# Kernel tuning notes

Hardware: AMD Instinct MI355X
Metric: run time of the kernel (lower is better)

## Reference

```python
import jax, jax.numpy as jnp
import numpy as np

D = 1024      # total input features
R = 32        # number of ragged regions
RMAX = 32     # max region size (padding target)
HIDDEN = [128, 128]
H1, H2 = HIDDEN
B = 8192      # batch size


def _made_masks(r, rmax, hidden):
    """TFP AutoregressiveNetwork masks (left-to-right order, 'equal' hidden degrees,
    params=2, use_bias=False), zero-padded to rmax features."""
    order = np.arange(1, r + 1)
    degs = [order]
    for u in hidden:
        mn = min(int(degs[-1].min()), r - 1)
        degs.append(np.maximum(mn, np.ceil(np.arange(1, u + 1) * (r - 1) / float(u + 1)).astype(np.int64)))
    m1 = np.zeros((rmax, hidden[0]), bool)
    m1[:r] = degs[0][:, None] <= degs[1][None, :]
    m2 = degs[1][:, None] <= degs[2][None, :]
    mout = np.zeros((hidden[-1], rmax * 2), bool)
    out_deg = np.repeat(order, 2)  # output layout is feature-major: [feat, param]
    mout[:, :2 * r] = degs[-1][:, None] < out_deg[None, :]
    return m1, m2, mout


def setup_inputs() -> dict:
    rng = np.random.default_rng(0)
    perm = rng.permutation(D)
    sizes = rng.integers(8, RMAX + 1, size=R)
    idx = np.zeros((R, RMAX), np.int64)
    valid = np.zeros((R, RMAX), bool)
    M1 = np.zeros((R, RMAX, H1), bool)
    M2 = np.zeros((R, H1, H2), bool)
    Mout = np.zeros((R, H2, RMAX * 2), bool)
    pos = 0
    for i in range(R):
        s = int(sizes[i])
        idx[i, :s] = perm[pos:pos + s]
        pos += s
        valid[i, :s] = True
        M1[i], M2[i], Mout[i] = _made_masks(s, RMAX, HIDDEN)
    key = jax.random.key(0)
    k1, k2, k3, k4 = jax.random.split(key, 4)
    inputs = jax.random.normal(k1, (B, D), jnp.float32)
    W1 = jax.random.normal(k2, (R, RMAX, H1), jnp.float32) / np.float32(np.sqrt(RMAX))
    W2 = jax.random.normal(k3, (R, H1, H2), jnp.float32) / np.float32(np.sqrt(H1))
    Wout = jax.random.normal(k4, (R, H2, RMAX * 2), jnp.float32) / np.float32(np.sqrt(H2))
    return {"inputs": inputs, "W1": W1, "W2": W2, "Wout": Wout,
            "idx": jnp.asarray(idx), "valid": jnp.asarray(valid),
            "M1": jnp.asarray(M1), "M2": jnp.asarray(M2), "Mout": jnp.asarray(Mout)}


def reference(inputs, W1, W2, Wout, idx, valid, M1, M2, Mout):
    f = inputs.dtype
    v = valid.astype(f)                              # [R, RMAX]
    xg = jnp.take(inputs, idx, axis=1) * v           # [B, R, RMAX] ragged gather (padded)
    # MADE masked MLP (relu, no bias), batched over all regions at once
    h1 = jax.nn.relu(jnp.einsum('brd,rdh->brh', xg, W1 * M1.astype(f)))
    h2 = jax.nn.relu(jnp.einsum('brh,rhk->brk', h1, W2 * M2.astype(f)))
    out = jnp.einsum('brk,rko->bro', h2, Wout * Mout.astype(f))
    out = out.reshape(out.shape[0], out.shape[1], RMAX, 2)
    shift, log_s = out[..., 0], out[..., 1]
    # MAF inverse: u = (x - shift) * exp(-log_scale); logdet = -sum(log_scale)
    u = (xg - shift) * jnp.exp(-log_s)
    elem = -0.5 * u * u - 0.5 * jnp.log(2.0 * jnp.pi) - log_s
    ll = jnp.sum(elem * v, axis=-1)                  # [B, R]
    return ll[..., None]                             # [B, R, 1] as in tf.stack of expand_dims
```

## Files before the change

### kernel.cpp

```cpp
#include <hip/hip_runtime.h>
#include <math.h>


#define RR 32
#define DD 1024
#define HH 128
#define OO 64
#define TROWS 32
#define TILES_PER_BLOCK 16
#define BLOCKS_PER_R 16

#define SHP 136
#define SXG 40
#define SXF 38
#define SSC 132

typedef short bf16x8_t __attribute__((ext_vector_type(8)));
typedef float f32x4_t __attribute__((ext_vector_type(4)));
typedef unsigned short u16;
typedef unsigned int u32;

__device__ __forceinline__ u16 bf16_rne(float x) {
    u32 u = __float_as_uint(x);
    u += 0x7FFFu + ((u >> 16) & 1u);
    return (u16)(u >> 16);
}
__device__ __forceinline__ float bf16_tof(u16 h) {
    return __uint_as_float(((u32)h) << 16);
}
__device__ __forceinline__ u16 lo_trunc(float v, u16 h) {
    return (u16)(__float_as_uint(v - bf16_tof(h)) >> 16);
}
__device__ __forceinline__ u32 pack_split(float v) {
    u16 h = bf16_rne(v);
    return (u32)h | ((u32)lo_trunc(v, h) << 16);
}
__device__ __forceinline__ void unpack8(const u32* p, bf16x8_t& hi, bf16x8_t& lo) {
    uint4 a = *reinterpret_cast<const uint4*>(p);
    uint4 b = *reinterpret_cast<const uint4*>(p + 4);
    union { u32 u[4]; bf16x8_t v; } H, L;
    H.u[0] = __builtin_amdgcn_perm(a.y, a.x, 0x05040100u);
    H.u[1] = __builtin_amdgcn_perm(a.w, a.z, 0x05040100u);
    H.u[2] = __builtin_amdgcn_perm(b.y, b.x, 0x05040100u);
    H.u[3] = __builtin_amdgcn_perm(b.w, b.z, 0x05040100u);
    L.u[0] = __builtin_amdgcn_perm(a.y, a.x, 0x07060302u);
    L.u[1] = __builtin_amdgcn_perm(a.w, a.z, 0x07060302u);
    L.u[2] = __builtin_amdgcn_perm(b.y, b.x, 0x07060302u);
    L.u[3] = __builtin_amdgcn_perm(b.w, b.z, 0x07060302u);
    hi = H.v; lo = L.v;
}
__device__ __forceinline__ f32x4_t mfma16(bf16x8_t a, bf16x8_t b, f32x4_t c) {
    return __builtin_amdgcn_mfma_f32_16x16x32_bf16(a, b, c, 0, 0, 0);
}

__device__ __forceinline__ void stage_block(const float* __restrict__ W,
                                            const int* __restrict__ M,
                                            int ldc, int c0, int K, u32* dst, int sd,
                                            int tid)
{
    const int kb = tid >> 3;
    const int cb = tid & 7;
    if (kb * 4 >= K) return;
    const int k0 = kb * 4;
    float e[4][4];
#pragma unroll
    for (int i = 0; i < 4; ++i) {
        const int o = ((k0 + i) * ldc + c0 + 4 * cb) >> 2;
        float4 w = ((const float4*)W)[o];
        int4   m = ((const int4*)M)[o];
        e[i][0] = m.x ? w.x : 0.f; e[i][1] = m.y ? w.y : 0.f;
        e[i][2] = m.z ? w.z : 0.f; e[i][3] = m.w ? w.w : 0.f;
    }
#pragma unroll
    for (int j = 0; j < 4; ++j) {
        uint4 p;
        p.x = pack_split(e[0][j]); p.y = pack_split(e[1][j]);
        p.z = pack_split(e[2][j]); p.w = pack_split(e[3][j]);
        *(uint4*)&dst[(4 * cb + j) * sd + k0] = p;
    }
}

__global__ __launch_bounds__(256, 2)
void made_flow_r9(const float* __restrict__ inputs,
                  const float* __restrict__ W1,
                  const float* __restrict__ W2,
                  const float* __restrict__ Wout,
                  const int* __restrict__ idx,
                  const int* __restrict__ valid,
                  const int* __restrict__ M1,
                  const int* __restrict__ M2,
                  const int* __restrict__ Mout,
                  float* __restrict__ out)
{
    __shared__ __align__(16) char regA[TROWS * SHP * 2 * 2];
    __shared__ __align__(16) char regB[TROWS * SHP * 2 * 2];
    __shared__ __align__(16) u16  xgh[2][TROWS * SXG];
    __shared__ __align__(16) u16  xgl[2][TROWS * SXG];
    __shared__ __align__(16) float xgf[2][TROWS * SXF];
    __shared__ __align__(16) float red_all[TILES_PER_BLOCK][TROWS][4];
    __shared__ int   idx_s[RR];
    __shared__ float v_s[RR];

    u16* const h1h = (u16*)regA;
    u16* const h1l = h1h + TROWS * SHP;
    u32* const scr = (u32*)regA;
    u16* const h2h = (u16*)regB;
    u16* const h2l = h2h + TROWS * SHP;

    const int tid  = threadIdx.x;
    const int r    = blockIdx.x / BLOCKS_PER_R;
    const int rb   = blockIdx.x % BLOCKS_PER_R;
    const int lane = tid & 63;
    const int wave = tid >> 6;
    const int q    = lane >> 4;
    const int l16  = lane & 15;

    if (tid < RR) {
        idx_s[tid] = idx[r * RR + tid];
        v_s[tid]   = valid[r * RR + tid] ? 1.f : 0.f;
    }

    bf16x8_t a1h[2], a1l[2];
    bf16x8_t a2h[2][4], a2l[2][4];
    bf16x8_t aoh[4],    aol[4];
    {
        const float* W1r = W1 + r * RR * HH;   const int* M1r = M1 + r * RR * HH;
        const float* W2r = W2 + r * HH * HH;   const int* M2r = M2 + r * HH * HH;
        const float* Wor = Wout + r * HH * OO; const int* Mor = Mout + r * HH * OO;
        for (int c = 0; c < 4; ++c) {
            __syncthreads();
            stage_block(W2r, M2r, HH, 32 * c, HH, scr, SSC, tid);
            __syncthreads();
            if (wave == c) {
#pragma unroll
                for (int mi = 0; mi < 2; ++mi)
#pragma unroll
                    for (int ks = 0; ks < 4; ++ks)
                        unpack8(&scr[(16 * mi + l16) * SSC + ks * 32 + q * 8],
                                a2h[mi][ks], a2l[mi][ks]);
            }
        }
        for (int c = 0; c < 2; ++c) {
            __syncthreads();
            stage_block(Wor, Mor, OO, 32 * c, HH, scr, SSC, tid);
            __syncthreads();
            if ((wave >> 1) == c) {
                const int nl = wave & 1;
#pragma unroll
                for (int ks = 0; ks < 4; ++ks)
                    unpack8(&scr[(16 * nl + l16) * SSC + ks * 32 + q * 8],
                            aoh[ks], aol[ks]);
            }
        }
        for (int c = 0; c < 4; ++c) {
            __syncthreads();
            stage_block(W1r, M1r, HH, 32 * c, RR, scr, SSC, tid);
            __syncthreads();
            if (wave == c) {
#pragma unroll
                for (int mi = 0; mi < 2; ++mi)
                    unpack8(&scr[(16 * mi + l16) * SSC + q * 8], a1h[mi], a1l[mi]);
            }
        }
    }
    __syncthreads();

    const f32x4_t zero4 = {0.f, 0.f, 0.f, 0.f};
    const int grow = tid >> 3, gg = tid & 7;

    {
        const int base = (rb * TILES_PER_BLOCK * TROWS + grow) * DD;
        float gx[4];
#pragma unroll
        for (int u = 0; u < 4; ++u)
            gx[u] = inputs[base + idx_s[4 * gg + u]] * v_s[4 * gg + u];
        ushort4 gh, gl;
        gh.x = bf16_rne(gx[0]); gl.x = lo_trunc(gx[0], gh.x);
        gh.y = bf16_rne(gx[1]); gl.y = lo_trunc(gx[1], gh.y);
        gh.z = bf16_rne(gx[2]); gl.z = lo_trunc(gx[2], gh.z);
        gh.w = bf16_rne(gx[3]); gl.w = lo_trunc(gx[3], gh.w);
        *(ushort4*)&xgh[0][grow * SXG + 4 * gg] = gh;
        *(ushort4*)&xgl[0][grow * SXG + 4 * gg] = gl;
        *(float2*)&xgf[0][grow * SXF + 4 * gg]     = make_float2(gx[0], gx[1]);
        *(float2*)&xgf[0][grow * SXF + 4 * gg + 2] = make_float2(gx[2], gx[3]);
    }
    __syncthreads();

    {
        bf16x8_t bh[2], bl[2];
#pragma unroll
        for (int ni = 0; ni < 2; ++ni) {
            bh[ni] = *(const bf16x8_t*)&xgh[0][(16 * ni + l16) * SXG + q * 8];
            bl[ni] = *(const bf16x8_t*)&xgl[0][(16 * ni + l16) * SXG + q * 8];
        }
#pragma unroll
        for (int mi = 0; mi < 2; ++mi)
#pragma unroll
            for (int ni = 0; ni < 2; ++ni) {
                f32x4_t a = zero4;
                a = mfma16(a1h[mi], bh[ni], a);
                a = mfma16(a1l[mi], bh[ni], a);
                a = mfma16(a1h[mi], bl[ni], a);
                ushort4 vh, vl;
                float v0 = fmaxf(a[0], 0.f), v1 = fmaxf(a[1], 0.f);
                float v2 = fmaxf(a[2], 0.f), v3 = fmaxf(a[3], 0.f);
                vh.x = bf16_rne(v0); vl.x = lo_trunc(v0, vh.x);
                vh.y = bf16_rne(v1); vl.y = lo_trunc(v1, vh.y);
                vh.z = bf16_rne(v2); vl.z = lo_trunc(v2, vh.z);
                vh.w = bf16_rne(v3); vl.w = lo_trunc(v3, vh.w);
                const int o = (16 * ni + l16) * SHP + 32 * wave + 16 * mi + 4 * q;
                *(ushort4*)&h1h[o] = vh;
                *(ushort4*)&h1l[o] = vl;
            }
    }

    for (int t = 0; t < TILES_PER_BLOCK; ++t) {
        const int row0 = (rb * TILES_PER_BLOCK + t) * TROWS;
        __syncthreads();

        float gx[4];
        const bool dg = (t + 1 < TILES_PER_BLOCK);
        if (dg) {
            const int base = (row0 + TROWS + grow) * DD;
#pragma unroll
            for (int u = 0; u < 4; ++u)
                gx[u] = inputs[base + idx_s[4 * gg + u]] * v_s[4 * gg + u];
        }
        {
            f32x4_t acc[2][2] = {{zero4, zero4}, {zero4, zero4}};
#pragma unroll
            for (int ks = 0; ks < 4; ++ks) {
#pragma unroll
                for (int ni = 0; ni < 2; ++ni) {
                    bf16x8_t bh = *(const bf16x8_t*)&h1h[(16 * ni + l16) * SHP + ks * 32 + q * 8];
                    bf16x8_t bl = *(const bf16x8_t*)&h1l[(16 * ni + l16) * SHP + ks * 32 + q * 8];
#pragma unroll
                    for (int mi = 0; mi < 2; ++mi) {
                        f32x4_t a = acc[mi][ni];
                        a = mfma16(a2h[mi][ks], bh, a);
                        a = mfma16(a2l[mi][ks], bh, a);
                        a = mfma16(a2h[mi][ks], bl, a);
                        acc[mi][ni] = a;
                    }
                }
            }
            if (dg) {
                const int b = (t + 1) & 1;
                ushort4 gh, gl;
                gh.x = bf16_rne(gx[0]); gl.x = lo_trunc(gx[0], gh.x);
                gh.y = bf16_rne(gx[1]); gl.y = lo_trunc(gx[1], gh.y);
                gh.z = bf16_rne(gx[2]); gl.z = lo_trunc(gx[2], gh.z);
                gh.w = bf16_rne(gx[3]); gl.w = lo_trunc(gx[3], gh.w);
                *(ushort4*)&xgh[b][grow * SXG + 4 * gg] = gh;
                *(ushort4*)&xgl[b][grow * SXG + 4 * gg] = gl;
                *(float2*)&xgf[b][grow * SXF + 4 * gg]     = make_float2(gx[0], gx[1]);
                *(float2*)&xgf[b][grow * SXF + 4 * gg + 2] = make_float2(gx[2], gx[3]);
            }
#pragma unroll
            for (int mi = 0; mi < 2; ++mi)
#pragma unroll
                for (int ni = 0; ni < 2; ++ni) {
                    ushort4 vh, vl;
                    float v0 = fmaxf(acc[mi][ni][0], 0.f), v1 = fmaxf(acc[mi][ni][1], 0.f);
                    float v2 = fmaxf(acc[mi][ni][2], 0.f), v3 = fmaxf(acc[mi][ni][3], 0.f);
                    vh.x = bf16_rne(v0); vl.x = lo_trunc(v0, vh.x);
                    vh.y = bf16_rne(v1); vl.y = lo_trunc(v1, vh.y);
                    vh.z = bf16_rne(v2); vl.z = lo_trunc(v2, vh.z);
                    vh.w = bf16_rne(v3); vl.w = lo_trunc(v3, vh.w);
                    const int o = (16 * ni + l16) * SHP + 32 * wave + 16 * mi + 4 * q;
                    *(ushort4*)&h2h[o] = vh;
                    *(ushort4*)&h2l[o] = vl;
                }
        }
        __syncthreads();

        f32x4_t acc3[2] = {zero4, zero4};
#pragma unroll
        for (int ks = 0; ks < 4; ++ks) {
#pragma unroll
            for (int ni = 0; ni < 2; ++ni) {
                bf16x8_t bh = *(const bf16x8_t*)&h2h[(16 * ni + l16) * SHP + ks * 32 + q * 8];
                bf16x8_t bl = *(const bf16x8_t*)&h2l[(16 * ni + l16) * SHP + ks * 32 + q * 8];
                f32x4_t a = acc3[ni];
                a = mfma16(aoh[ks], bh, a);
                a = mfma16(aol[ks], bh, a);
                a = mfma16(aoh[ks], bl, a);
                acc3[ni] = a;
            }
        }

        if (dg) {
            const int b = (t + 1) & 1;
            bf16x8_t bh[2], bl[2];
#pragma unroll
            for (int ni = 0; ni < 2; ++ni) {
                bh[ni] = *(const bf16x8_t*)&xgh[b][(16 * ni + l16) * SXG + q * 8];
                bl[ni] = *(const bf16x8_t*)&xgl[b][(16 * ni + l16) * SXG + q * 8];
            }
#pragma unroll
            for (int mi = 0; mi < 2; ++mi)
#pragma unroll
                for (int ni = 0; ni < 2; ++ni) {
                    f32x4_t a = zero4;
                    a = mfma16(a1h[mi], bh[ni], a);
                    a = mfma16(a1l[mi], bh[ni], a);
                    a = mfma16(a1h[mi], bl[ni], a);
                    ushort4 vh, vl;
                    float v0 = fmaxf(a[0], 0.f), v1 = fmaxf(a[1], 0.f);
                    float v2 = fmaxf(a[2], 0.f), v3 = fmaxf(a[3], 0.f);
                    vh.x = bf16_rne(v0); vl.x = lo_trunc(v0, vh.x);
                    vh.y = bf16_rne(v1); vl.y = lo_trunc(v1, vh.y);
                    vh.z = bf16_rne(v2); vl.z = lo_trunc(v2, vh.z);
                    vh.w = bf16_rne(v3); vl.w = lo_trunc(v3, vh.w);
                    const int o = (16 * ni + l16) * SHP + 32 * wave + 16 * mi + 4 * q;
                    *(ushort4*)&h1h[o] = vh;
                    *(ushort4*)&h1l[o] = vl;
                }
        }

        {
            const int j0 = 8 * wave + 2 * q;
            const float vj0 = v_s[j0], vj1 = v_s[j0 + 1];
            float p[2];
#pragma unroll
            for (int ni = 0; ni < 2; ++ni) {
                const int row = 16 * ni + l16;
                float2 xv = *(const float2*)&xgf[t & 1][row * SXF + j0];
                const float u0 = (xv.x - acc3[ni][0]) * __expf(-acc3[ni][1]);
                const float u1 = (xv.y - acc3[ni][2]) * __expf(-acc3[ni][3]);
                p[ni] = (-0.5f * u0 * u0 - 0.91893853320467266954f - acc3[ni][1]) * vj0
                      + (-0.5f * u1 * u1 - 0.91893853320467266954f - acc3[ni][3]) * vj1;
            }
#pragma unroll
            for (int ni = 0; ni < 2; ++ni) {
                p[ni] += __shfl_xor(p[ni], 16, 64);
                p[ni] += __shfl_xor(p[ni], 32, 64);
            }
            if (q == 0) {
#pragma unroll
                for (int ni = 0; ni < 2; ++ni)
                    red_all[t][16 * ni + l16][wave] = p[ni];
            }
        }
    }

    __syncthreads();
#pragma unroll
    for (int rep = 0; rep < 2; ++rep) {
        const int f   = tid + rep * 256;
        const int tt  = f >> 5;
        const int row = f & 31;
        float4 rv = *(const float4*)&red_all[tt][row][0];
        out[((rb * TILES_PER_BLOCK + tt) * TROWS + row) * RR + r] =
            rv.x + rv.y + rv.z + rv.w;
    }
}

extern "C" void kernel_launch(void* const* d_in, const int* in_sizes, int n_in,
                              void* d_out, int out_size, void* d_ws, size_t ws_size,
                              hipStream_t stream)
{
    const float* inputs = (const float*)d_in[0];
    const float* W1     = (const float*)d_in[1];
    const float* W2     = (const float*)d_in[2];
    const float* Wout   = (const float*)d_in[3];
    const int*   idx    = (const int*)d_in[4];
    const int*   valid  = (const int*)d_in[5];
    const int*   M1     = (const int*)d_in[6];
    const int*   M2     = (const int*)d_in[7];
    const int*   Mout   = (const int*)d_in[8];
    float*       out    = (float*)d_out;

    hipLaunchKernelGGL(made_flow_r9, dim3(RR * BLOCKS_PER_R), dim3(256), 0, stream,
                       inputs, W1, W2, Wout, idx, valid, M1, M2, Mout, out);
}
```

Before: 143.6 us.

## Software-pipeline MLP layers across tiles with one barrier and swizzled LDS

Restructures the per-tile loop into a skewed pipeline: layer 2 of tile t, layer 1 of tile t+1 and the output layer plus likelihood of tile t-1 run in the same iteration, with double-buffered h1/h2. This drops one __syncthreads per tile. Padded LDS strides become XOR-swizzled layouts, and the fp32 xg buffer is replaced by re-reading inputs from global memory at the output stage. Per-tile results are written out inside the loop, so the large reduction buffer goes away. The cost is extra global gathers and more complex indexing.

```diff
diff --git a/kernel.cpp b/kernel.cpp
--- a/kernel.cpp
+++ b/kernel.cpp
@@ -7,12 +7,11 @@
 #define HH 128
 #define OO 64
 #define TROWS 32
-#define TILES_PER_BLOCK 16
-#define BLOCKS_PER_R 16
-
-#define SHP 136
-#define SXG 40
-#define SXF 38
+#define TILES 16
+#define BPR 16
+
+#define SH  128
+#define SX  32
 #define SSC 132
 
 typedef short bf16x8_t __attribute__((ext_vector_type(8)));
@@ -52,6 +51,12 @@
 __device__ __forceinline__ f32x4_t mfma16(bf16x8_t a, bf16x8_t b, f32x4_t c) {
     return __builtin_amdgcn_mfma_f32_16x16x32_bf16(a, b, c, 0, 0, 0);
 }
+__device__ __forceinline__ int hsw(int row, int col) {
+    return row * SH + (col ^ (16 * (row & 7)));
+}
+__device__ __forceinline__ int xsw(int row, int col) {
+    return row * SX + (col ^ (8 * (row & 3)));
+}
 
 __device__ __forceinline__ void stage_block(const float* __restrict__ W,
                                             const int* __restrict__ M,
@@ -81,35 +86,29 @@
 }
 
 __global__ __launch_bounds__(256, 2)
-void made_flow_r9(const float* __restrict__ inputs,
-                  const float* __restrict__ W1,
-                  const float* __restrict__ W2,
-                  const float* __restrict__ Wout,
-                  const int* __restrict__ idx,
-                  const int* __restrict__ valid,
-                  const int* __restrict__ M1,
-                  const int* __restrict__ M2,
-                  const int* __restrict__ Mout,
-                  float* __restrict__ out)
+void made_flow_r10(const float* __restrict__ inputs,
+                   const float* __restrict__ W1,
+                   const float* __restrict__ W2,
+                   const float* __restrict__ Wout,
+                   const int* __restrict__ idx,
+                   const int* __restrict__ valid,
+                   const int* __restrict__ M1,
+                   const int* __restrict__ M2,
+                   const int* __restrict__ Mout,
+                   float* __restrict__ out)
 {
-    __shared__ __align__(16) char regA[TROWS * SHP * 2 * 2];
-    __shared__ __align__(16) char regB[TROWS * SHP * 2 * 2];
-    __shared__ __align__(16) u16  xgh[2][TROWS * SXG];
-    __shared__ __align__(16) u16  xgl[2][TROWS * SXG];
-    __shared__ __align__(16) float xgf[2][TROWS * SXF];
-    __shared__ __align__(16) float red_all[TILES_PER_BLOCK][TROWS][4];
+    __shared__ __align__(16) u16 h1p[2][2][TROWS * SH];
+    __shared__ __align__(16) u16 h2p[2][2][TROWS * SH];
+    __shared__ __align__(16) u16 xgp[2][2][TROWS * SX];
+    __shared__ __align__(16) float red[2][TROWS][4];
     __shared__ int   idx_s[RR];
     __shared__ float v_s[RR];
 
-    u16* const h1h = (u16*)regA;
-    u16* const h1l = h1h + TROWS * SHP;
-    u32* const scr = (u32*)regA;
-    u16* const h2h = (u16*)regB;
-    u16* const h2l = h2h + TROWS * SHP;
+    u32* const scr = (u32*)&h1p[0][0][0];
 
     const int tid  = threadIdx.x;
-    const int r    = blockIdx.x / BLOCKS_PER_R;
-    const int rb   = blockIdx.x % BLOCKS_PER_R;
+    const int r    = blockIdx.x / BPR;
+    const int rb   = blockIdx.x % BPR;
     const int lane = tid & 63;
     const int wave = tid >> 6;
     const int q    = lane >> 4;
@@ -163,13 +162,14 @@
             }
         }
     }
-    __syncthreads();
 
     const f32x4_t zero4 = {0.f, 0.f, 0.f, 0.f};
     const int grow = tid >> 3, gg = tid & 7;
-
-    {
-        const int base = (rb * TILES_PER_BLOCK * TROWS + grow) * DD;
+    const int row0g = rb * TILES * TROWS;
+
+#pragma unroll
+    for (int tt = 0; tt < 2; ++tt) {
+        const int base = (row0g + tt * TROWS + grow) * DD;
         float gx[4];
 #pragma unroll
         for (int u = 0; u < 4; ++u)
@@ -179,10 +179,9 @@
         gh.y = bf16_rne(gx[1]); gl.y = lo_trunc(gx[1], gh.y);
         gh.z = bf16_rne(gx[2]); gl.z = lo_trunc(gx[2], gh.z);
         gh.w = bf16_rne(gx[3]); gl.w = lo_trunc(gx[3], gh.w);
-        *(ushort4*)&xgh[0][grow * SXG + 4 * gg] = gh;
-        *(ushort4*)&xgl[0][grow * SXG + 4 * gg] = gl;
-        *(float2*)&xgf[0][grow * SXF + 4 * gg]     = make_float2(gx[0], gx[1]);
-        *(float2*)&xgf[0][grow * SXF + 4 * gg + 2] = make_float2(gx[2], gx[3]);
+        const int o = xsw(grow, 4 * gg);
+        *(ushort4*)&xgp[tt][0][o] = gh;
+        *(ushort4*)&xgp[tt][1][o] = gl;
     }
     __syncthreads();
 
@@ -190,8 +189,9 @@
         bf16x8_t bh[2], bl[2];
 #pragma unroll
         for (int ni = 0; ni < 2; ++ni) {
-            bh[ni] = *(const bf16x8_t*)&xgh[0][(16 * ni + l16) * SXG + q * 8];
-            bl[ni] = *(const bf16x8_t*)&xgl[0][(16 * ni + l16) * SXG + q * 8];
+            const int o = xsw(16 * ni + l16, q * 8);
+            bh[ni] = *(const bf16x8_t*)&xgp[0][0][o];
+            bl[ni] = *(const bf16x8_t*)&xgp[0][1][o];
         }
 #pragma unroll
         for (int mi = 0; mi < 2; ++mi)
@@ -208,32 +208,56 @@
                 vh.y = bf16_rne(v1); vl.y = lo_trunc(v1, vh.y);
                 vh.z = bf16_rne(v2); vl.z = lo_trunc(v2, vh.z);
                 vh.w = bf16_rne(v3); vl.w = lo_trunc(v3, vh.w);
-                const int o = (16 * ni + l16) * SHP + 32 * wave + 16 * mi + 4 * q;
-                *(ushort4*)&h1h[o] = vh;
-                *(ushort4*)&h1l[o] = vl;
-            }
-    }
-
-    for (int t = 0; t < TILES_PER_BLOCK; ++t) {
-        const int row0 = (rb * TILES_PER_BLOCK + t) * TROWS;
+                const int o = hsw(16 * ni + l16, 32 * wave + 16 * mi + 4 * q);
+                *(ushort4*)&h1p[0][0][o] = vh;
+                *(ushort4*)&h1p[0][1][o] = vl;
+            }
+    }
+
+    for (int t = 0; t <= TILES + 1; ++t) {
         __syncthreads();
 
+        if (t >= 2 && tid < TROWS) {
+            float4 rv = *(const float4*)&red[t & 1][tid][0];
+            out[((rb * TILES + (t - 2)) * TROWS + tid) * RR + r] =
+                rv.x + rv.y + rv.z + rv.w;
+        }
+
         float gx[4];
-        const bool dg = (t + 1 < TILES_PER_BLOCK);
+        const bool dg = (t + 2 < TILES);
         if (dg) {
-            const int base = (row0 + TROWS + grow) * DD;
+            const int base = (row0g + (t + 2) * TROWS + grow) * DD;
 #pragma unroll
             for (int u = 0; u < 4; ++u)
                 gx[u] = inputs[base + idx_s[4 * gg + u]] * v_s[4 * gg + u];
         }
-        {
+        float ex[4];
+        const int j0 = 8 * wave + 2 * q;
+        const bool de = (t >= 1 && t <= TILES);
+        if (de) {
+            const int baseE = (row0g + (t - 1) * TROWS) * DD;
+#pragma unroll
+            for (int ni = 0; ni < 2; ++ni)
+#pragma unroll
+                for (int jj = 0; jj < 2; ++jj)
+                    ex[2 * ni + jj] =
+                        inputs[(baseE + (16 * ni + l16) * DD) + idx_s[j0 + jj]] *
+                        v_s[j0 + jj];
+        }
+
+        if (t < TILES) {
+            const u16* h1h = h1p[t & 1][0];
+            const u16* h1l = h1p[t & 1][1];
+            u16* const h2h = h2p[t & 1][0];
+            u16* const h2l = h2p[t & 1][1];
             f32x4_t acc[2][2] = {{zero4, zero4}, {zero4, zero4}};
 #pragma unroll
             for (int ks = 0; ks < 4; ++ks) {
 #pragma unroll
                 for (int ni = 0; ni < 2; ++ni) {
-                    bf16x8_t bh = *(const bf16x8_t*)&h1h[(16 * ni + l16) * SHP + ks * 32 + q * 8];
-                    bf16x8_t bl = *(const bf16x8_t*)&h1l[(16 * ni + l16) * SHP + ks * 32 + q * 8];
+                    const int o = hsw(16 * ni + l16, ks * 32 + q * 8);
+                    bf16x8_t bh = *(const bf16x8_t*)&h1h[o];
+                    bf16x8_t bl = *(const bf16x8_t*)&h1l[o];
 #pragma unroll
                     for (int mi = 0; mi < 2; ++mi) {
                         f32x4_t a = acc[mi][ni];
@@ -244,18 +268,6 @@
                     }
                 }
             }
-            if (dg) {
-                const int b = (t + 1) & 1;
-                ushort4 gh, gl;
-                gh.x = bf16_rne(gx[0]); gl.x = lo_trunc(gx[0], gh.x);
-                gh.y = bf16_rne(gx[1]); gl.y = lo_trunc(gx[1], gh.y);
-                gh.z = bf16_rne(gx[2]); gl.z = lo_trunc(gx[2], gh.z);
-                gh.w = bf16_rne(gx[3]); gl.w = lo_trunc(gx[3], gh.w);
-                *(ushort4*)&xgh[b][grow * SXG + 4 * gg] = gh;
-                *(ushort4*)&xgl[b][grow * SXG + 4 * gg] = gl;
-                *(float2*)&xgf[b][grow * SXF + 4 * gg]     = make_float2(gx[0], gx[1]);
-                *(float2*)&xgf[b][grow * SXF + 4 * gg + 2] = make_float2(gx[2], gx[3]);
-            }
 #pragma unroll
             for (int mi = 0; mi < 2; ++mi)
 #pragma unroll
@@ -267,35 +279,20 @@
                     vh.y = bf16_rne(v1); vl.y = lo_trunc(v1, vh.y);
                     vh.z = bf16_rne(v2); vl.z = lo_trunc(v2, vh.z);
                     vh.w = bf16_rne(v3); vl.w = lo_trunc(v3, vh.w);
-                    const int o = (16 * ni + l16) * SHP + 32 * wave + 16 * mi + 4 * q;
+                    const int o = hsw(16 * ni + l16, 32 * wave + 16 * mi + 4 * q);
                     *(ushort4*)&h2h[o] = vh;
                     *(ushort4*)&h2l[o] = vl;
                 }
         }
-        __syncthreads();
-
-        f32x4_t acc3[2] = {zero4, zero4};
-#pragma unroll
-        for (int ks = 0; ks < 4; ++ks) {
-#pragma unroll
-            for (int ni = 0; ni < 2; ++ni) {
-                bf16x8_t bh = *(const bf16x8_t*)&h2h[(16 * ni + l16) * SHP + ks * 32 + q * 8];
-                bf16x8_t bl = *(const bf16x8_t*)&h2l[(16 * ni + l16) * SHP + ks * 32 + q * 8];
-                f32x4_t a = acc3[ni];
-                a = mfma16(aoh[ks], bh, a);
-                a = mfma16(aol[ks], bh, a);
-                a = mfma16(aoh[ks], bl, a);
-                acc3[ni] = a;
-            }
-        }
-
-        if (dg) {
+
+        if (t + 1 < TILES) {
             const int b = (t + 1) & 1;
             bf16x8_t bh[2], bl[2];
 #pragma unroll
             for (int ni = 0; ni < 2; ++ni) {
-                bh[ni] = *(const bf16x8_t*)&xgh[b][(16 * ni + l16) * SXG + q * 8];
-                bl[ni] = *(const bf16x8_t*)&xgl[b][(16 * ni + l16) * SXG + q * 8];
+                const int o = xsw(16 * ni + l16, q * 8);
+                bh[ni] = *(const bf16x8_t*)&xgp[b][0][o];
+                bl[ni] = *(const bf16x8_t*)&xgp[b][1][o];
             }
 #pragma unroll
             for (int mi = 0; mi < 2; ++mi)
@@ -312,22 +309,48 @@
                     vh.y = bf16_rne(v1); vl.y = lo_trunc(v1, vh.y);
                     vh.z = bf16_rne(v2); vl.z = lo_trunc(v2, vh.z);
                     vh.w = bf16_rne(v3); vl.w = lo_trunc(v3, vh.w);
-                    const int o = (16 * ni + l16) * SHP + 32 * wave + 16 * mi + 4 * q;
-                    *(ushort4*)&h1h[o] = vh;
-                    *(ushort4*)&h1l[o] = vl;
+                    const int o = hsw(16 * ni + l16, 32 * wave + 16 * mi + 4 * q);
+                    *(ushort4*)&h1p[b][0][o] = vh;
+                    *(ushort4*)&h1p[b][1][o] = vl;
                 }
         }
 
-        {
-            const int j0 = 8 * wave + 2 * q;
+        if (dg) {
+            ushort4 gh, gl;
+            gh.x = bf16_rne(gx[0]); gl.x = lo_trunc(gx[0], gh.x);
+            gh.y = bf16_rne(gx[1]); gl.y = lo_trunc(gx[1], gh.y);
+            gh.z = bf16_rne(gx[2]); gl.z = lo_trunc(gx[2], gh.z);
+            gh.w = bf16_rne(gx[3]); gl.w = lo_trunc(gx[3], gh.w);
+            const int o = xsw(grow, 4 * gg);
+            *(ushort4*)&xgp[t & 1][0][o] = gh;
+            *(ushort4*)&xgp[t & 1][1][o] = gl;
+        }
+
+        if (de) {
+            const int tm = t - 1;
+            const u16* h2h = h2p[tm & 1][0];
+            const u16* h2l = h2p[tm & 1][1];
+            f32x4_t acc3[2] = {zero4, zero4};
+#pragma unroll
+            for (int ks = 0; ks < 4; ++ks) {
+#pragma unroll
+                for (int ni = 0; ni < 2; ++ni) {
+                    const int o = hsw(16 * ni + l16, ks * 32 + q * 8);
+                    bf16x8_t bh = *(const bf16x8_t*)&h2h[o];
+                    bf16x8_t bl = *(const bf16x8_t*)&h2l[o];
+                    f32x4_t a = acc3[ni];
+                    a = mfma16(aoh[ks], bh, a);
+                    a = mfma16(aol[ks], bh, a);
+                    a = mfma16(aoh[ks], bl, a);
+                    acc3[ni] = a;
+                }
+            }
             const float vj0 = v_s[j0], vj1 = v_s[j0 + 1];
             float p[2];
 #pragma unroll
             for (int ni = 0; ni < 2; ++ni) {
-                const int row = 16 * ni + l16;
-                float2 xv = *(const float2*)&xgf[t & 1][row * SXF + j0];
-                const float u0 = (xv.x - acc3[ni][0]) * __expf(-acc3[ni][1]);
-                const float u1 = (xv.y - acc3[ni][2]) * __expf(-acc3[ni][3]);
+                const float u0 = (ex[2 * ni + 0] - acc3[ni][0]) * __expf(-acc3[ni][1]);
+                const float u1 = (ex[2 * ni + 1] - acc3[ni][2]) * __expf(-acc3[ni][3]);
                 p[ni] = (-0.5f * u0 * u0 - 0.91893853320467266954f - acc3[ni][1]) * vj0
                       + (-0.5f * u1 * u1 - 0.91893853320467266954f - acc3[ni][3]) * vj1;
             }
@@ -339,20 +362,9 @@
             if (q == 0) {
 #pragma unroll
                 for (int ni = 0; ni < 2; ++ni)
-                    red_all[t][16 * ni + l16][wave] = p[ni];
-            }
-        }
-    }
-
-    __syncthreads();
-#pragma unroll
-    for (int rep = 0; rep < 2; ++rep) {
-        const int f   = tid + rep * 256;
-        const int tt  = f >> 5;
-        const int row = f & 31;
-        float4 rv = *(const float4*)&red_all[tt][row][0];
-        out[((rb * TILES_PER_BLOCK + tt) * TROWS + row) * RR + r] =
-            rv.x + rv.y + rv.z + rv.w;
+                    red[tm & 1][16 * ni + l16][wave] = p[ni];
+            }
+        }
     }
 }
 
@@ -371,6 +383,6 @@
     const int*   Mout   = (const int*)d_in[8];
     float*       out    = (float*)d_out;
 
-    hipLaunchKernelGGL(made_flow_r9, dim3(RR * BLOCKS_PER_R), dim3(256), 0, stream,
+    hipLaunchKernelGGL(made_flow_r10, dim3(RR * BPR), dim3(256), 0, stream,
                        inputs, W1, W2, Wout, idx, valid, M1, M2, Mout, out);
 }
```

After: 159.6 us. +11.1%, slower.

## Double grid, swizzle hidden LDS planes, drop fp32 xg copy, raise occupancy

Applied to the files above, without the earlier changes.

The grid is doubled to 32 blocks per region, each handling 8 row tiles instead of 16, and launch bounds are raised to 3 blocks per CU. The padded hidden-activation planes are replaced with unpadded XOR-swizzled planes, and the fp32 copy of the gathered input is removed, with x rebuilt from its bf16 hi/lo split. Together these shrink LDS use and aim to raise occupancy and reduce bank conflicts. The trade-off is that the per-region weight staging into registers is now amortised over half as many tiles, and the rebuilt x differs slightly in precision from the original fp32 value.

```diff
diff --git a/kernel.cpp b/kernel.cpp
--- a/kernel.cpp
+++ b/kernel.cpp
@@ -7,12 +7,11 @@
 #define HH 128
 #define OO 64
 #define TROWS 32
-#define TILES_PER_BLOCK 16
-#define BLOCKS_PER_R 16
-
-#define SHP 136
+#define TILES 8
+#define BPR 32
+
+#define SH  128
 #define SXG 40
-#define SXF 38
 #define SSC 132
 
 typedef short bf16x8_t __attribute__((ext_vector_type(8)));
@@ -52,6 +51,9 @@
 __device__ __forceinline__ f32x4_t mfma16(bf16x8_t a, bf16x8_t b, f32x4_t c) {
     return __builtin_amdgcn_mfma_f32_16x16x32_bf16(a, b, c, 0, 0, 0);
 }
+__device__ __forceinline__ int hsw(int row, int col) {
+    return row * SH + (col ^ (16 * (row & 7)));
+}
 
 __device__ __forceinline__ void stage_block(const float* __restrict__ W,
                                             const int* __restrict__ M,
@@ -80,36 +82,34 @@
     }
 }
 
-__global__ __launch_bounds__(256, 2)
-void made_flow_r9(const float* __restrict__ inputs,
-                  const float* __restrict__ W1,
-                  const float* __restrict__ W2,
-                  const float* __restrict__ Wout,
-                  const int* __restrict__ idx,
-                  const int* __restrict__ valid,
-                  const int* __restrict__ M1,
-                  const int* __restrict__ M2,
-                  const int* __restrict__ Mout,
-                  float* __restrict__ out)
+__global__ __launch_bounds__(256, 3)
+void made_flow_r11(const float* __restrict__ inputs,
+                   const float* __restrict__ W1,
+                   const float* __restrict__ W2,
+                   const float* __restrict__ Wout,
+                   const int* __restrict__ idx,
+                   const int* __restrict__ valid,
+                   const int* __restrict__ M1,
+                   const int* __restrict__ M2,
+                   const int* __restrict__ Mout,
+                   float* __restrict__ out)
 {
-    __shared__ __align__(16) char regA[TROWS * SHP * 2 * 2];
-    __shared__ __align__(16) char regB[TROWS * SHP * 2 * 2];
-    __shared__ __align__(16) u16  xgh[2][TROWS * SXG];
-    __shared__ __align__(16) u16  xgl[2][TROWS * SXG];
-    __shared__ __align__(16) float xgf[2][TROWS * SXF];
-    __shared__ __align__(16) float red_all[TILES_PER_BLOCK][TROWS][4];
+    __shared__ __align__(16) u16 hplanes[2][2][TROWS * SH];
+    __shared__ __align__(16) u16 xgh[2][TROWS * SXG];
+    __shared__ __align__(16) u16 xgl[2][TROWS * SXG];
+    __shared__ __align__(16) float red_all[TILES][TROWS][4];
     __shared__ int   idx_s[RR];
     __shared__ float v_s[RR];
 
-    u16* const h1h = (u16*)regA;
-    u16* const h1l = h1h + TROWS * SHP;
-    u32* const scr = (u32*)regA;
-    u16* const h2h = (u16*)regB;
-    u16* const h2l = h2h + TROWS * SHP;
+    u16* const h1h = hplanes[0][0];
+    u16* const h1l = hplanes[0][1];
+    u16* const h2h = hplanes[1][0];
+    u16* const h2l = hplanes[1][1];
+    u32* const scr = (u32*)hplanes;
 
     const int tid  = threadIdx.x;
-    const int r    = blockIdx.x / BLOCKS_PER_R;
-    const int rb   = blockIdx.x % BLOCKS_PER_R;
+    const int r    = blockIdx.x / BPR;
+    const int rb   = blockIdx.x % BPR;
     const int lane = tid & 63;
     const int wave = tid >> 6;
     const int q    = lane >> 4;
@@ -167,9 +167,10 @@
 
     const f32x4_t zero4 = {0.f, 0.f, 0.f, 0.f};
     const int grow = tid >> 3, gg = tid & 7;
+    const int row0g = rb * TILES * TROWS;
 
     {
-        const int base = (rb * TILES_PER_BLOCK * TROWS + grow) * DD;
+        const int base = (row0g + grow) * DD;
         float gx[4];
 #pragma unroll
         for (int u = 0; u < 4; ++u)
@@ -181,8 +182,6 @@
         gh.w = bf16_rne(gx[3]); gl.w = lo_trunc(gx[3], gh.w);
         *(ushort4*)&xgh[0][grow * SXG + 4 * gg] = gh;
         *(ushort4*)&xgl[0][grow * SXG + 4 * gg] = gl;
-        *(float2*)&xgf[0][grow * SXF + 4 * gg]     = make_float2(gx[0], gx[1]);
-        *(float2*)&xgf[0][grow * SXF + 4 * gg + 2] = make_float2(gx[2], gx[3]);
     }
     __syncthreads();
 
@@ -190,8 +189,9 @@
         bf16x8_t bh[2], bl[2];
 #pragma unroll
         for (int ni = 0; ni < 2; ++ni) {
-            bh[ni] = *(const bf16x8_t*)&xgh[0][(16 * ni + l16) * SXG + q * 8];
-            bl[ni] = *(const bf16x8_t*)&xgl[0][(16 * ni + l16) * SXG + q * 8];
+            const int o = (16 * ni + l16) * SXG + q * 8;
+            bh[ni] = *(const bf16x8_t*)&xgh[0][o];
+            bl[ni] = *(const bf16x8_t*)&xgl[0][o];
         }
 #pragma unroll
         for (int mi = 0; mi < 2; ++mi)
@@ -208,20 +208,19 @@
                 vh.y = bf16_rne(v1); vl.y = lo_trunc(v1, vh.y);
                 vh.z = bf16_rne(v2); vl.z = lo_trunc(v2, vh.z);
                 vh.w = bf16_rne(v3); vl.w = lo_trunc(v3, vh.w);
-                const int o = (16 * ni + l16) * SHP + 32 * wave + 16 * mi + 4 * q;
+                const int o = hsw(16 * ni + l16, 32 * wave + 16 * mi + 4 * q);
                 *(ushort4*)&h1h[o] = vh;
                 *(ushort4*)&h1l[o] = vl;
             }
     }
 
-    for (int t = 0; t < TILES_PER_BLOCK; ++t) {
-        const int row0 = (rb * TILES_PER_BLOCK + t) * TROWS;
+    for (int t = 0; t < TILES; ++t) {
         __syncthreads();
 
         float gx[4];
-        const bool dg = (t + 1 < TILES_PER_BLOCK);
+        const bool dg = (t + 1 < TILES);
         if (dg) {
-            const int base = (row0 + TROWS + grow) * DD;
+            const int base = (row0g + (t + 1) * TROWS + grow) * DD;
 #pragma unroll
             for (int u = 0; u < 4; ++u)
                 gx[u] = inputs[base + idx_s[4 * gg + u]] * v_s[4 * gg + u];
@@ -232,8 +231,9 @@
             for (int ks = 0; ks < 4; ++ks) {
 #pragma unroll
                 for (int ni = 0; ni < 2; ++ni) {
-                    bf16x8_t bh = *(const bf16x8_t*)&h1h[(16 * ni + l16) * SHP + ks * 32 + q * 8];
-                    bf16x8_t bl = *(const bf16x8_t*)&h1l[(16 * ni + l16) * SHP + ks * 32 + q * 8];
+                    const int o = hsw(16 * ni + l16, ks * 32 + q * 8);
+                    bf16x8_t bh = *(const bf16x8_t*)&h1h[o];
+                    bf16x8_t bl = *(const bf16x8_t*)&h1l[o];
 #pragma unroll
                     for (int mi = 0; mi < 2; ++mi) {
                         f32x4_t a = acc[mi][ni];
@@ -253,8 +253,6 @@
                 gh.w = bf16_rne(gx[3]); gl.w = lo_trunc(gx[3], gh.w);
                 *(ushort4*)&xgh[b][grow * SXG + 4 * gg] = gh;
                 *(ushort4*)&xgl[b][grow * SXG + 4 * gg] = gl;
-                *(float2*)&xgf[b][grow * SXF + 4 * gg]     = make_float2(gx[0], gx[1]);
-                *(float2*)&xgf[b][grow * SXF + 4 * gg + 2] = make_float2(gx[2], gx[3]);
             }
 #pragma unroll
             for (int mi = 0; mi < 2; ++mi)
@@ -267,7 +265,7 @@
                     vh.y = bf16_rne(v1); vl.y = lo_trunc(v1, vh.y);
                     vh.z = bf16_rne(v2); vl.z = lo_trunc(v2, vh.z);
                     vh.w = bf16_rne(v3); vl.w = lo_trunc(v3, vh.w);
-                    const int o = (16 * ni + l16) * SHP + 32 * wave + 16 * mi + 4 * q;
+                    const int o = hsw(16 * ni + l16, 32 * wave + 16 * mi + 4 * q);
                     *(ushort4*)&h2h[o] = vh;
                     *(ushort4*)&h2l[o] = vl;
                 }
@@ -279,8 +277,9 @@
         for (int ks = 0; ks < 4; ++ks) {
 #pragma unroll
             for (int ni = 0; ni < 2; ++ni) {
-                bf16x8_t bh = *(const bf16x8_t*)&h2h[(16 * ni + l16) * SHP + ks * 32 + q * 8];
-                bf16x8_t bl = *(const bf16x8_t*)&h2l[(16 * ni + l16) * SHP + ks * 32 + q * 8];
+                const int o = hsw(16 * ni + l16, ks * 32 + q * 8);
+                bf16x8_t bh = *(const bf16x8_t*)&h2h[o];
+                bf16x8_t bl = *(const bf16x8_t*)&h2l[o];
                 f32x4_t a = acc3[ni];
                 a = mfma16(aoh[ks], bh, a);
                 a = mfma16(aol[ks], bh, a);
@@ -294,8 +293,9 @@
             bf16x8_t bh[2], bl[2];
 #pragma unroll
             for (int ni = 0; ni < 2; ++ni) {
-                bh[ni] = *(const bf16x8_t*)&xgh[b][(16 * ni + l16) * SXG + q * 8];
-                bl[ni] = *(const bf16x8_t*)&xgl[b][(16 * ni + l16) * SXG + q * 8];
+                const int o = (16 * ni + l16) * SXG + q * 8;
+                bh[ni] = *(const bf16x8_t*)&xgh[b][o];
+                bl[ni] = *(const bf16x8_t*)&xgl[b][o];
             }
 #pragma unroll
             for (int mi = 0; mi < 2; ++mi)
@@ -312,7 +312,7 @@
                     vh.y = bf16_rne(v1); vl.y = lo_trunc(v1, vh.y);
                     vh.z = bf16_rne(v2); vl.z = lo_trunc(v2, vh.z);
                     vh.w = bf16_rne(v3); vl.w = lo_trunc(v3, vh.w);
-                    const int o = (16 * ni + l16) * SHP + 32 * wave + 16 * mi + 4 * q;
+                    const int o = hsw(16 * ni + l16, 32 * wave + 16 * mi + 4 * q);
                     *(ushort4*)&h1h[o] = vh;
                     *(ushort4*)&h1l[o] = vl;
                 }
@@ -325,9 +325,13 @@
 #pragma unroll
             for (int ni = 0; ni < 2; ++ni) {
                 const int row = 16 * ni + l16;
-                float2 xv = *(const float2*)&xgf[t & 1][row * SXF + j0];
-                const float u0 = (xv.x - acc3[ni][0]) * __expf(-acc3[ni][1]);
-                const float u1 = (xv.y - acc3[ni][2]) * __expf(-acc3[ni][3]);
+                const u32 hx = *(const u32*)&xgh[t & 1][row * SXG + j0];
+                const u32 lx = *(const u32*)&xgl[t & 1][row * SXG + j0];
+                const float x0 = __uint_as_float(hx << 16) + __uint_as_float(lx << 16);
+                const float x1 = __uint_as_float(hx & 0xFFFF0000u) +
+                                 __uint_as_float(lx & 0xFFFF0000u);
+                const float u0 = (x0 - acc3[ni][0]) * __expf(-acc3[ni][1]);
+                const float u1 = (x1 - acc3[ni][2]) * __expf(-acc3[ni][3]);
                 p[ni] = (-0.5f * u0 * u0 - 0.91893853320467266954f - acc3[ni][1]) * vj0
                       + (-0.5f * u1 * u1 - 0.91893853320467266954f - acc3[ni][3]) * vj1;
             }
@@ -345,13 +349,11 @@
     }
 
     __syncthreads();
-#pragma unroll
-    for (int rep = 0; rep < 2; ++rep) {
-        const int f   = tid + rep * 256;
-        const int tt  = f >> 5;
-        const int row = f & 31;
+    {
+        const int tt  = tid >> 5;
+        const int row = tid & 31;
         float4 rv = *(const float4*)&red_all[tt][row][0];
-        out[((rb * TILES_PER_BLOCK + tt) * TROWS + row) * RR + r] =
+        out[((rb * TILES + tt) * TROWS + row) * RR + r] =
             rv.x + rv.y + rv.z + rv.w;
     }
 }
@@ -371,6 +373,6 @@
     const int*   Mout   = (const int*)d_in[8];
     float*       out    = (float*)d_out;
 
-    hipLaunchKernelGGL(made_flow_r9, dim3(RR * BLOCKS_PER_R), dim3(256), 0, stream,
+    hipLaunchKernelGGL(made_flow_r11, dim3(RR * BPR), dim3(256), 0, stream,
                        inputs, W1, W2, Wout, idx, valid, M1, M2, Mout, out);
 }
```

Measured after the change: 161.1 us. +12.2%, slower.
